# Kernel optimization log

Hardware: AMD Instinct MI355X
Metric: run time of the kernel (lower is better)

## Reference

```python
import jax, jax.numpy as jnp
import numpy as np

ANG = 9        # angRes (forced by hardcoded center index 40 -> 81 views)
MINDISP = -4
MAXDISP = 4


def setup_inputs() -> dict:
    key = jax.random.key(0)
    k1, k2 = jax.random.split(key)
    x = jax.random.normal(k1, (2, 4, 81, 96, 96), dtype=jnp.float32)
    mask = jax.random.uniform(k2, (2, 81, 96, 96), dtype=jnp.float32)
    return {"x": x, "mask": mask}


def _build_cost(x, mask):
    # Faithful translation of BuildCost.forward.
    # The chain of (ZeroPad2d on each view) -> (macro-image rearrange) ->
    # (crop) -> (Unfold kernel=A, dilation=(h_pad-d, w_pad-d)) -> (mask
    # modulate) -> (Unfold2) is algebraically a per-view shifted gather:
    #   cost[b,d,p,q,ck,u,v] = x_padview[b,ck,u,v, p+off(d,u), q+off(d,v)]
    #                          * mask[b, u*A+v, p, q]
    # with off(d,t) = (A//2)*(d-mindisp) - t*d, on views zero-padded by
    # bdr = (A//2)*maxdisp. Unfold2 is a pure reshape of the modulated
    # unfold columns. All indices stay inside each padded view.
    A, mind, maxd = ANG, MINDISP, MAXDISP
    b, c, aa, h, w = x.shape
    ctr = x[:, :, 40:41, :, :]                       # [b, c, 1, h, w]
    c0 = A // 2
    bdr = c0 * maxd
    xv = x.reshape(b, c, A, A, h, w)
    xp = jnp.pad(xv, ((0, 0), (0, 0), (0, 0), (0, 0), (bdr, bdr), (bdr, bdr)))
    D = maxd - mind + 1
    d = jnp.arange(mind, maxd + 1)                   # [D]
    uv = jnp.arange(A)                               # [A]
    off = c0 * (d[:, None] - mind) - uv[None, :] * d[:, None]   # [D, A]
    ridx = off[:, :, None] + jnp.arange(h)[None, None, :]       # [D, A, h]
    cidx = off[:, :, None] + jnp.arange(w)[None, None, :]       # [D, A, w]
    ui = uv[None, :, None, None, None]               # broadcast to [D,A,A,h,w]
    vi = uv[None, None, :, None, None]
    ri = ridx[:, :, None, :, None]
    ci = cidx[:, None, :, None, :]
    # g[b, c, D, u, v, p, q]
    g = xp[:, :, ui, vi, ri, ci]
    m = mask.reshape(b, 1, 1, A, A, h, w)            # mask channel a = u*A+v
    cost = g * m
    # torch output layout: [b, D, (p*w+q)*c + ck, u*A+v]
    cost = cost.transpose(0, 2, 5, 6, 1, 3, 4).reshape(b, D, h * w * c, A * A)
    return cost, ctr


def reference(x, mask):
    return _build_cost(x, mask)
```

## Files before the change

kernel.cpp:

```cpp
#include <hip/hip_runtime.h>


#define NAA 81
#define H 96
#define W 96
#define NC 4
#define ND 9
#define PLANE 9216
#define NR 324
#define RS 324
#define JB 32
#define OUTROW 31104
#define CTR_OFF 53747712LL
#define XTOT 5971968

typedef float f32x4 __attribute__((ext_vector_type(4)));
typedef f32x4 __attribute__((aligned(4))) f32x4u;

__global__ __launch_bounds__(512, 6)
void build_cost_kernel(const float* __restrict__ x, const float* __restrict__ mask,
                       float* __restrict__ out) {
    __shared__ __align__(16) float xs[JB * RS];
    __shared__ __align__(16) int   lut[2 * NR];

    const int ii  = blockIdx.x;
    const int dd  = blockIdx.y;
    const int zz  = blockIdx.z;
    const int b   = zz / 3;
    const int jc  = zz - 3 * b;
    const int j0  = JB * jc;
    const int d   = dd - 4;
    const int tid = threadIdx.x;

    if (tid < NR) {
        int row = tid;
        int c  = row / 81;
        int uv = row - 81 * c;
        int u  = uv / 9;
        int v  = uv - 9 * u;
        int ri = ii + d * (4 - u);
        int xb = ((b * NC + c) * NAA + uv) * PLANE + ri * W;
        int mb = ((b * NAA + uv) * H + ii) * W;
        int s  = d * (4 - v);
        lut[2 * tid]     = ((unsigned)ri < (unsigned)H) ? xb : -1;
        lut[2 * tid + 1] = (mb << 6) | (s + 16);
    }
    __syncthreads();

    for (int idx = tid; idx < NAA * 8; idx += 512) {
        int rq = idx >> 3;
        int j4 = idx & 7;
        int jb = 4 * j4;
        int4 P0 = *(const int4*)&lut[8 * rq];
        int4 P1 = *(const int4*)&lut[8 * rq + 4];

        auto ld = [&](int xb, int B) -> f32x4 {
            int s    = (B & 63) - 16;
            int col0 = j0 + jb + s;
            int a0   = xb + col0;
            int addr = min(max(a0, 0), XTOT - 4);
            f32x4 xv = *(const f32x4u*)(x + addr);
            f32x4 mv = *(const f32x4*)(mask + (B >> 6) + j0 + jb);
            f32x4 r;
            bool rv = (xb >= 0);
            r.x = (rv && (unsigned)(col0 + 0) < (unsigned)W) ? xv.x * mv.x : 0.0f;
            r.y = (rv && (unsigned)(col0 + 1) < (unsigned)W) ? xv.y * mv.y : 0.0f;
            r.z = (rv && (unsigned)(col0 + 2) < (unsigned)W) ? xv.z * mv.z : 0.0f;
            r.w = (rv && (unsigned)(col0 + 3) < (unsigned)W) ? xv.w * mv.w : 0.0f;
            return r;
        };

        f32x4 v0 = ld(P0.x, P0.y);
        f32x4 v1 = ld(P0.z, P0.w);
        f32x4 v2 = ld(P1.x, P1.y);
        f32x4 v3 = ld(P1.z, P1.w);

        float* base = &xs[4 * rq];
        f32x4 w0 = {v0.x, v1.x, v2.x, v3.x};
        f32x4 w1 = {v0.y, v1.y, v2.y, v3.y};
        f32x4 w2 = {v0.z, v1.z, v2.z, v3.z};
        f32x4 w3 = {v0.w, v1.w, v2.w, v3.w};
        *(f32x4*)(base + (jb + 0) * RS) = w0;
        *(f32x4*)(base + (jb + 1) * RS) = w1;
        *(f32x4*)(base + (jb + 2) * RS) = w2;
        *(f32x4*)(base + (jb + 3) * RS) = w3;
    }
    __syncthreads();

    const size_t obase = (size_t)((b * ND + dd) * H + ii) * OUTROW + (size_t)j0 * NR;
    for (int idx = tid; idx < NAA * JB; idx += 512) {
        f32x4 v = *(const f32x4*)&xs[4 * idx];
        __builtin_nontemporal_store(v, (f32x4*)(out + obase + 4 * (size_t)idx));
    }

    if (dd == 4 && jc == 0 && tid < 96) {
        int c = tid / 24;
        int q = tid - 24 * c;
        size_t so  = (size_t)((b * NC + c) * NAA + 40) * PLANE + (size_t)ii * W + 4 * q;
        size_t dst = CTR_OFF + (size_t)((b * NC + c) * H + ii) * W + 4 * q;
        f32x4 cv = *(const f32x4*)(x + so);
        __builtin_nontemporal_store(cv, (f32x4*)(out + dst));
    }
}

extern "C" void kernel_launch(void* const* d_in, const int* in_sizes, int n_in,
                              void* d_out, int out_size, void* d_ws, size_t ws_size,
                              hipStream_t stream) {
    const float* x    = (const float*)d_in[0];
    const float* mask = (const float*)d_in[1];
    float* out = (float*)d_out;
    dim3 grid(96, ND, 6);
    build_cost_kernel<<<grid, 512, 0, stream>>>(x, mask, out);
}
```

Baseline: 259.0 us.

## Give each wave a private LDS slice and software-pipeline gather loads with stores

Each block now covers the full output row (all 96 columns) instead of a third of it. The block is split into 4 waves, and each wave owns a private 8-column LDS slice that it fills and drains three times, syncing only at the wave level. The global gather loads for the next slice are issued before the current slice is stored out, so load latency overlaps with the nontemporal stores and the block-wide barrier between phases goes away. In exchange, occupancy and grid size drop (256 threads, a grid 3x smaller) and register pressure rises from the prefetched vectors.

Result: slower. 274.8 us (+6.1%).

```diff
diff --git a/kernel.cpp b/kernel.cpp
--- a/kernel.cpp
+++ b/kernel.cpp
@@ -8,8 +8,8 @@
 #define ND 9
 #define PLANE 9216
 #define NR 324
-#define RS 324
-#define JB 32
+#define JBW 8
+#define SLICE (JBW * NR)
 #define OUTROW 31104
 #define CTR_OFF 53747712LL
 #define XTOT 5971968
@@ -17,23 +17,36 @@
 typedef float f32x4 __attribute__((ext_vector_type(4)));
 typedef f32x4 __attribute__((aligned(4))) f32x4u;
 
-__global__ __launch_bounds__(512, 6)
+#define WAVE_SYNC() do { \
+    asm volatile("s_waitcnt lgkmcnt(0)" ::: "memory"); \
+    __builtin_amdgcn_wave_barrier(); \
+} while (0)
+
+__device__ __forceinline__ f32x4 combine(f32x4 xv, f32x4 mv, int xb, int col0) {
+    f32x4 r;
+    bool rv = xb >= 0;
+    r.x = (rv && (unsigned)(col0 + 0) < (unsigned)W) ? xv.x * mv.x : 0.0f;
+    r.y = (rv && (unsigned)(col0 + 1) < (unsigned)W) ? xv.y * mv.y : 0.0f;
+    r.z = (rv && (unsigned)(col0 + 2) < (unsigned)W) ? xv.z * mv.z : 0.0f;
+    r.w = (rv && (unsigned)(col0 + 3) < (unsigned)W) ? xv.w * mv.w : 0.0f;
+    return r;
+}
+
+__global__ __launch_bounds__(256, 3)
 void build_cost_kernel(const float* __restrict__ x, const float* __restrict__ mask,
                        float* __restrict__ out) {
-    __shared__ __align__(16) float xs[JB * RS];
+    __shared__ __align__(16) float xs[4 * SLICE];
     __shared__ __align__(16) int   lut[2 * NR];
 
     const int ii  = blockIdx.x;
     const int dd  = blockIdx.y;
-    const int zz  = blockIdx.z;
-    const int b   = zz / 3;
-    const int jc  = zz - 3 * b;
-    const int j0  = JB * jc;
+    const int b   = blockIdx.z;
     const int d   = dd - 4;
     const int tid = threadIdx.x;
+    const int w    = tid >> 6;
+    const int lane = tid & 63;
 
-    if (tid < NR) {
-        int row = tid;
+    for (int row = tid; row < NR; row += 256) {
         int c  = row / 81;
         int uv = row - 81 * c;
         int u  = uv / 9;
@@ -42,64 +55,132 @@
         int xb = ((b * NC + c) * NAA + uv) * PLANE + ri * W;
         int mb = ((b * NAA + uv) * H + ii) * W;
         int s  = d * (4 - v);
-        lut[2 * tid]     = ((unsigned)ri < (unsigned)H) ? xb : -1;
-        lut[2 * tid + 1] = (mb << 6) | (s + 16);
+        lut[2 * row]     = ((unsigned)ri < (unsigned)H) ? xb : -1;
+        lut[2 * row + 1] = (mb << 6) | (s + 16);
     }
     __syncthreads();
 
-    for (int idx = tid; idx < NAA * 8; idx += 512) {
-        int rq = idx >> 3;
-        int j4 = idx & 7;
-        int jb = 4 * j4;
-        int4 P0 = *(const int4*)&lut[8 * rq];
-        int4 P1 = *(const int4*)&lut[8 * rq + 4];
-
-        auto ld = [&](int xb, int B) -> f32x4 {
-            int s    = (B & 63) - 16;
-            int col0 = j0 + jb + s;
-            int a0   = xb + col0;
-            int addr = min(max(a0, 0), XTOT - 4);
-            f32x4 xv = *(const f32x4u*)(x + addr);
-            f32x4 mv = *(const f32x4*)(mask + (B >> 6) + j0 + jb);
-            f32x4 r;
-            bool rv = (xb >= 0);
-            r.x = (rv && (unsigned)(col0 + 0) < (unsigned)W) ? xv.x * mv.x : 0.0f;
-            r.y = (rv && (unsigned)(col0 + 1) < (unsigned)W) ? xv.y * mv.y : 0.0f;
-            r.z = (rv && (unsigned)(col0 + 2) < (unsigned)W) ? xv.z * mv.z : 0.0f;
-            r.w = (rv && (unsigned)(col0 + 3) < (unsigned)W) ? xv.w * mv.w : 0.0f;
-            return r;
-        };
-
-        f32x4 v0 = ld(P0.x, P0.y);
-        f32x4 v1 = ld(P0.z, P0.w);
-        f32x4 v2 = ld(P1.x, P1.y);
-        f32x4 v3 = ld(P1.z, P1.w);
-
-        float* base = &xs[4 * rq];
-        f32x4 w0 = {v0.x, v1.x, v2.x, v3.x};
-        f32x4 w1 = {v0.y, v1.y, v2.y, v3.y};
-        f32x4 w2 = {v0.z, v1.z, v2.z, v3.z};
-        f32x4 w3 = {v0.w, v1.w, v2.w, v3.w};
-        *(f32x4*)(base + (jb + 0) * RS) = w0;
-        *(f32x4*)(base + (jb + 1) * RS) = w1;
-        *(f32x4*)(base + (jb + 2) * RS) = w2;
-        *(f32x4*)(base + (jb + 3) * RS) = w3;
-    }
-    __syncthreads();
-
-    const size_t obase = (size_t)((b * ND + dd) * H + ii) * OUTROW + (size_t)j0 * NR;
-    for (int idx = tid; idx < NAA * JB; idx += 512) {
-        f32x4 v = *(const f32x4*)&xs[4 * idx];
-        __builtin_nontemporal_store(v, (f32x4*)(out + obase + 4 * (size_t)idx));
-    }
-
-    if (dd == 4 && jc == 0 && tid < 96) {
+    if (dd == 4 && tid < 96) {
         int c = tid / 24;
         int q = tid - 24 * c;
         size_t so  = (size_t)((b * NC + c) * NAA + 40) * PLANE + (size_t)ii * W + 4 * q;
         size_t dst = CTR_OFF + (size_t)((b * NC + c) * H + ii) * W + 4 * q;
         f32x4 cv = *(const f32x4*)(x + so);
         __builtin_nontemporal_store(cv, (f32x4*)(out + dst));
+    }
+
+    float* const slice = &xs[w * SLICE];
+    const size_t obase = (size_t)((b * ND + dd) * H + ii) * OUTROW;
+
+    const int rq0 = lane >> 1;
+    const int jh  = lane & 1;
+    const int rq1 = rq0 + 32;
+    const int rq2 = rq0 + 64;
+    const bool has2 = (lane < 34);
+
+    f32x4 xr0[4], xr1[4];
+
+    auto issue = [&](int j0w) {
+        int jb = j0w + 4 * jh;
+        {
+            int4 P0 = *(const int4*)&lut[8 * rq0];
+            int4 P1 = *(const int4*)&lut[8 * rq0 + 4];
+            xr0[0] = *(const f32x4u*)(x + min(max(P0.x + jb + ((P0.y & 63) - 16), 0), XTOT - 4));
+            xr0[1] = *(const f32x4u*)(x + min(max(P0.z + jb + ((P0.w & 63) - 16), 0), XTOT - 4));
+            xr0[2] = *(const f32x4u*)(x + min(max(P1.x + jb + ((P1.y & 63) - 16), 0), XTOT - 4));
+            xr0[3] = *(const f32x4u*)(x + min(max(P1.z + jb + ((P1.w & 63) - 16), 0), XTOT - 4));
+        }
+        {
+            int4 P0 = *(const int4*)&lut[8 * rq1];
+            int4 P1 = *(const int4*)&lut[8 * rq1 + 4];
+            xr1[0] = *(const f32x4u*)(x + min(max(P0.x + jb + ((P0.y & 63) - 16), 0), XTOT - 4));
+            xr1[1] = *(const f32x4u*)(x + min(max(P0.z + jb + ((P0.w & 63) - 16), 0), XTOT - 4));
+            xr1[2] = *(const f32x4u*)(x + min(max(P1.x + jb + ((P1.y & 63) - 16), 0), XTOT - 4));
+            xr1[3] = *(const f32x4u*)(x + min(max(P1.z + jb + ((P1.w & 63) - 16), 0), XTOT - 4));
+        }
+    };
+
+    auto cw = [&](int rq, int jb, const f32x4* xv) {
+        int4 P0 = *(const int4*)&lut[8 * rq];
+        int4 P1 = *(const int4*)&lut[8 * rq + 4];
+        f32x4 m0 = *(const f32x4*)(mask + (P0.y >> 6) + jb);
+        f32x4 m1 = *(const f32x4*)(mask + (P0.w >> 6) + jb);
+        f32x4 m2 = *(const f32x4*)(mask + (P1.y >> 6) + jb);
+        f32x4 m3 = *(const f32x4*)(mask + (P1.w >> 6) + jb);
+        f32x4 v0 = combine(xv[0], m0, P0.x, jb + ((P0.y & 63) - 16));
+        f32x4 v1 = combine(xv[1], m1, P0.z, jb + ((P0.w & 63) - 16));
+        f32x4 v2 = combine(xv[2], m2, P1.x, jb + ((P1.y & 63) - 16));
+        f32x4 v3 = combine(xv[3], m3, P1.z, jb + ((P1.w & 63) - 16));
+        float* bp = slice + 4 * rq + (4 * jh) * NR;
+        f32x4 t0 = {v0.x, v1.x, v2.x, v3.x};
+        f32x4 t1 = {v0.y, v1.y, v2.y, v3.y};
+        f32x4 t2 = {v0.z, v1.z, v2.z, v3.z};
+        f32x4 t3 = {v0.w, v1.w, v2.w, v3.w};
+        *(f32x4*)(bp + 0 * NR) = t0;
+        *(f32x4*)(bp + 1 * NR) = t1;
+        *(f32x4*)(bp + 2 * NR) = t2;
+        *(f32x4*)(bp + 3 * NR) = t3;
+    };
+
+    issue(8 * w);
+
+    #pragma unroll
+    for (int k = 0; k < 3; ++k) {
+        const int j0w = 8 * (w + 4 * k);
+        const int jb  = j0w + 4 * jh;
+
+        f32x4 a0, a1, a2, a3;
+        int4 Q0, Q1;
+        if (has2) {
+            Q0 = *(const int4*)&lut[8 * rq2];
+            Q1 = *(const int4*)&lut[8 * rq2 + 4];
+            a0 = *(const f32x4u*)(x + min(max(Q0.x + jb + ((Q0.y & 63) - 16), 0), XTOT - 4));
+            a1 = *(const f32x4u*)(x + min(max(Q0.z + jb + ((Q0.w & 63) - 16), 0), XTOT - 4));
+            a2 = *(const f32x4u*)(x + min(max(Q1.x + jb + ((Q1.y & 63) - 16), 0), XTOT - 4));
+            a3 = *(const f32x4u*)(x + min(max(Q1.z + jb + ((Q1.w & 63) - 16), 0), XTOT - 4));
+        }
+
+        cw(rq0, jb, xr0);
+        cw(rq1, jb, xr1);
+
+        if (has2) {
+            f32x4 m0 = *(const f32x4*)(mask + (Q0.y >> 6) + jb);
+            f32x4 m1 = *(const f32x4*)(mask + (Q0.w >> 6) + jb);
+            f32x4 m2 = *(const f32x4*)(mask + (Q1.y >> 6) + jb);
+            f32x4 m3 = *(const f32x4*)(mask + (Q1.w >> 6) + jb);
+            f32x4 v0 = combine(a0, m0, Q0.x, jb + ((Q0.y & 63) - 16));
+            f32x4 v1 = combine(a1, m1, Q0.z, jb + ((Q0.w & 63) - 16));
+            f32x4 v2 = combine(a2, m2, Q1.x, jb + ((Q1.y & 63) - 16));
+            f32x4 v3 = combine(a3, m3, Q1.z, jb + ((Q1.w & 63) - 16));
+            float* bp = slice + 4 * rq2 + (4 * jh) * NR;
+            f32x4 t0 = {v0.x, v1.x, v2.x, v3.x};
+            f32x4 t1 = {v0.y, v1.y, v2.y, v3.y};
+            f32x4 t2 = {v0.z, v1.z, v2.z, v3.z};
+            f32x4 t3 = {v0.w, v1.w, v2.w, v3.w};
+            *(f32x4*)(bp + 0 * NR) = t0;
+            *(f32x4*)(bp + 1 * NR) = t1;
+            *(f32x4*)(bp + 2 * NR) = t2;
+            *(f32x4*)(bp + 3 * NR) = t3;
+        }
+
+        WAVE_SYNC();
+
+        if (k < 2) issue(8 * (w + 4 * (k + 1)));
+
+        const size_t cb = obase + (size_t)j0w * NR;
+        #pragma unroll 2
+        for (int m2 = 0; m2 < 10; ++m2) {
+            int idx = lane + 64 * m2;
+            f32x4 v = *(const f32x4*)(slice + 4 * idx);
+            __builtin_nontemporal_store(v, (f32x4*)(out + cb + 4 * (size_t)idx));
+        }
+        if (lane < 8) {
+            int idx = lane + 640;
+            f32x4 v = *(const f32x4*)(slice + 4 * idx);
+            __builtin_nontemporal_store(v, (f32x4*)(out + cb + 4 * (size_t)idx));
+        }
+
+        WAVE_SYNC();
     }
 }
 
@@ -109,6 +190,6 @@
     const float* x    = (const float*)d_in[0];
     const float* mask = (const float*)d_in[1];
     float* out = (float*)d_out;
-    dim3 grid(96, ND, 6);
-    build_cost_kernel<<<grid, 512, 0, stream>>>(x, mask, out);
+    dim3 grid(96, ND, 2);
+    build_cost_kernel<<<grid, 256, 0, stream>>>(x, mask, out);
 }
```
